# Kernel optimization log

Hardware: AMD Instinct MI355X
Metric: run time of the kernel (lower is better)

Reference implementation:

```python
import jax, jax.numpy as jnp
import numpy as np

B, CQ, CKV, LQ, LKV, HEADS = 4, 1024, 1024, 2048, 2048, 16


def _conv1x1(W, x):
    # Conv1d with kernel size 1: out[b,o,l] = sum_i W[o,i] * x[b,i,l]
    return jnp.einsum('oi,bil->bol', W, x)


def _linear_interp(x, L_out):
    # F.interpolate(mode='linear', align_corners=False) on (B,C,L)
    B_, C_, L_in = x.shape
    if L_in == L_out:
        return x
    scale = L_in / L_out
    pos = (jnp.arange(L_out, dtype=x.dtype) + 0.5) * scale - 0.5
    pos = jnp.clip(pos, 0.0, L_in - 1)
    lo = jnp.floor(pos).astype(jnp.int32)
    hi = jnp.minimum(lo + 1, L_in - 1)
    w = (pos - lo.astype(x.dtype))
    return x[:, :, lo] * (1.0 - w) + x[:, :, hi] * w


def setup_inputs() -> dict:
    key = jax.random.key(0)
    ks = jax.random.split(key, 7)
    winit = 1.0 / np.sqrt(CQ)
    return {
        'query': jax.random.normal(ks[0], (B, CQ, LQ), dtype=jnp.float32),
        'context': jax.random.normal(ks[1], (B, CKV, LKV), dtype=jnp.float32),
        'Wq': jax.random.normal(ks[2], (CQ, CQ), dtype=jnp.float32) * winit,
        'Wk': jax.random.normal(ks[3], (CQ, CKV), dtype=jnp.float32) * winit,
        'Wv': jax.random.normal(ks[4], (CQ, CKV), dtype=jnp.float32) * winit,
        'Wo': jax.random.normal(ks[5], (CQ, CQ), dtype=jnp.float32) * winit,
        'bo': jnp.zeros((CQ,), dtype=jnp.float32),
        'heads': HEADS,
    }


def reference(query, context, Wq, Wk, Wv, Wo, bo, heads):
    B_, Cq, Lq = query.shape
    H = heads
    D = Cq // H
    scale = D ** (-0.5)
    q = _conv1x1(Wq, query).reshape(B_, H, D, Lq)
    k = _conv1x1(Wk, context)
    v = _conv1x1(Wv, context)
    if k.shape[2] != Lq:
        k = _linear_interp(k, Lq)
        v = _linear_interp(v, Lq)
    k = k.reshape(B_, H, D, Lq)
    v = v.reshape(B_, H, D, Lq)
    attn = jnp.einsum('bhdi,bhdj->bhij', q, k) * scale
    attn = jax.nn.softmax(attn, axis=-1)
    out = jnp.einsum('bhij,bhdj->bhdi', attn, v).reshape(B_, Cq, Lq)
    return _conv1x1(Wo, out) + bo[None, :, None] + query
```

## Files before the change

### kernel.cpp

```cpp
#include <hip/hip_runtime.h>
#include <hip/hip_bf16.h>

typedef __bf16 bf16;
typedef __attribute__((ext_vector_type(8))) __bf16 bf16x8;
typedef __attribute__((ext_vector_type(4))) __bf16 bf16x4;
typedef __attribute__((ext_vector_type(4))) float f32x4;
typedef __attribute__((ext_vector_type(8))) float f32x8;
typedef __attribute__((ext_vector_type(16))) float f32x16;
typedef unsigned int uint2v __attribute__((ext_vector_type(2)));

#define B_ 4
#define C_ 1024
#define L_ 2048
#define H_ 16
#define D_ 64

__device__ __forceinline__ int swz(int row, int g) {
    return row * 64 + (((g ^ row) & 7) << 3);
}

__device__ __forceinline__ void async_ld16(const bf16* g, bf16* l) {
    __builtin_amdgcn_global_load_lds(
        (const __attribute__((address_space(1))) unsigned int*)g,
        (__attribute__((address_space(3))) unsigned int*)l, 16, 0, 0);
}

__device__ __forceinline__ float fast_exp2(float x) {
    float r;
    asm("v_exp_f32 %0, %1" : "=v"(r) : "v"(x));
    return r;
}

__global__ void cvt_w4(const float* __restrict__ wq, const float* __restrict__ wk,
                       const float* __restrict__ wv, const float* __restrict__ wo,
                       bf16* __restrict__ oq, bf16* __restrict__ ok,
                       bf16* __restrict__ ov, bf16* __restrict__ oo,
                       float qscale) {
    int z = blockIdx.y;
    const float* in = (z == 0) ? wq : (z == 1) ? wk : (z == 2) ? wv : wo;
    bf16* out       = (z == 0) ? oq : (z == 1) ? ok : (z == 2) ? ov : oo;
    float scale     = (z == 0) ? qscale : 1.0f;
    int i = (blockIdx.x * blockDim.x + threadIdx.x) * 4;
    f32x4 x = *(const f32x4*)&in[i];
    bf16x4 y;
#pragma unroll
    for (int e = 0; e < 4; e++) y[e] = (bf16)(x[e] * scale);
    *(bf16x4*)&out[i] = y;
}

__global__ void transpose_cvt2(const float* __restrict__ q,
                               const float* __restrict__ c,
                               bf16* __restrict__ qo, bf16* __restrict__ co,
                               int nb) {
    __shared__ bf16 s[32][33];
    int z  = blockIdx.z;
    const float* pin;
    bf16* pout;
    if (z < nb) { pin = q + (size_t)z * C_ * L_;        pout = qo + (size_t)z * L_ * C_; }
    else        { pin = c + (size_t)(z - nb) * C_ * L_; pout = co + (size_t)(z - nb) * L_ * C_; }
    int c0 = blockIdx.x * 32;
    int r0 = blockIdx.y * 32;
#pragma unroll
    for (int k = 0; k < 4; k++) {
        int r = r0 + threadIdx.y + k * 8;
        s[threadIdx.y + k * 8][threadIdx.x] = (bf16)pin[(size_t)r * L_ + c0 + threadIdx.x];
    }
    __syncthreads();
#pragma unroll
    for (int k = 0; k < 4; k++) {
        int cc = c0 + threadIdx.y + k * 8;
        pout[(size_t)cc * C_ + r0 + threadIdx.x] = s[threadIdx.x][threadIdx.y + k * 8];
    }
}

__global__ __launch_bounds__(256) void gemm_fused3(const bf16* __restrict__ qT,
                                                   const bf16* __restrict__ ctxT,
                                                   const bf16* __restrict__ Wq,
                                                   const bf16* __restrict__ Wk,
                                                   const bf16* __restrict__ Wv,
                                                   bf16* __restrict__ qP,
                                                   bf16* __restrict__ kP,
                                                   bf16* __restrict__ vP,
                                                   int nb) {
    __shared__ __align__(16) bf16 smem[4 * 128 * 64];

    int seg = blockIdx.y;
    int r   = blockIdx.x;
    int cpx = nb << 4;
    int lg  = (r & 7) * cpx + (r >> 3);

    const bf16 *aP, *bP;
    bf16* dP;
    int S;
    if (seg == 0) {
        int m_idx = lg >> 3, n_idx = lg & 7;
        aP = qT + (size_t)m_idx * 128 * C_;
        bP = Wq + (size_t)n_idx * 128 * C_;
        dP = qP + (size_t)m_idx * 128 * C_ + n_idx * 128;
        S = C_;
    } else if (seg == 1) {
        int m_idx = lg >> 3, n_idx = lg & 7;
        aP = ctxT + (size_t)m_idx * 128 * C_;
        bP = Wk + (size_t)n_idx * 128 * C_;
        dP = kP + (size_t)m_idx * 128 * C_ + n_idx * 128;
        S = C_;
    } else {
        int m_idx = lg & 7;
        int nt    = lg >> 3;
        int zb    = nt >> 4;
        int nc0   = (nt & 15) * 128;
        aP = Wv + (size_t)m_idx * 128 * C_;
        bP = ctxT + (size_t)nt * 128 * C_;
        dP = vP + (size_t)zb * C_ * L_ + (size_t)m_idx * 128 * L_ + nc0;
        S = L_;
    }

    int t = threadIdx.x;
    int lane = t & 63, wave = t >> 6;
    int l15 = lane & 15, quad = lane >> 4;
    int wm = (wave >> 1) * 64, wn = (wave & 1) * 64;

    f32x4 acc[4][4];
#pragma unroll
    for (int i = 0; i < 4; i++)
#pragma unroll
        for (int j = 0; j < 4; j++) {
            f32x4 z = {0.f, 0.f, 0.f, 0.f};
            acc[i][j] = z;
        }

    int r8 = lane >> 3;
    int gl = (((lane & 7) ^ r8) & 7) * 8;
    const bf16* aG = aP + (size_t)(wave * 32 + r8) * C_ + gl;
    const bf16* wG = bP + (size_t)(wave * 32 + r8) * C_ + gl;

    auto STAGE = [&](int buf, int kk) {
        bf16* Ab = smem + buf * 8192;
        bf16* Wb = smem + 16384 + buf * 8192;
#pragma unroll
        for (int p = 0; p < 4; p++) {
            async_ld16(aG + kk + (size_t)p * 8 * C_, &Ab[(wave * 32 + p * 8) * 64]);
            async_ld16(wG + kk + (size_t)p * 8 * C_, &Wb[(wave * 32 + p * 8) * 64]);
        }
    };

    STAGE(0, 0);
    const int KT = C_ >> 6;
    for (int it = 0; it < KT; ++it) {
        int cur = it & 1;
        if (it + 1 < KT) {
            STAGE(cur ^ 1, (it + 1) << 6);
            asm volatile("s_waitcnt vmcnt(8)" ::: "memory");
        } else {
            asm volatile("s_waitcnt vmcnt(0)" ::: "memory");
        }
        __builtin_amdgcn_s_barrier();
        asm volatile("" ::: "memory");
        const bf16* Ab = smem + cur * 8192;
        const bf16* Wb = smem + 16384 + cur * 8192;
#pragma unroll
        for (int ks = 0; ks < 2; ks++) {
            bf16x8 af[4], bfr[4];
#pragma unroll
            for (int i = 0; i < 4; i++)
                af[i] = *(const bf16x8*)&Ab[swz(wm + i * 16 + l15, ks * 4 + quad)];
#pragma unroll
            for (int i = 0; i < 4; i++)
                bfr[i] = *(const bf16x8*)&Wb[swz(wn + i * 16 + l15, ks * 4 + quad)];
#pragma unroll
            for (int mt = 0; mt < 4; mt++)
#pragma unroll
                for (int nt2 = 0; nt2 < 4; nt2++)
                    acc[mt][nt2] = __builtin_amdgcn_mfma_f32_16x16x32_bf16(
                        af[mt], bfr[nt2], acc[mt][nt2], 0, 0, 0);
        }
        asm volatile("" ::: "memory");
        __builtin_amdgcn_s_barrier();
    }
    __syncthreads();

    bf16 (*Ts2)[136] = (bf16 (*)[136])smem;
#pragma unroll
    for (int mt = 0; mt < 4; mt++)
#pragma unroll
        for (int nt2 = 0; nt2 < 4; nt2++)
#pragma unroll
            for (int rr = 0; rr < 4; rr++)
                Ts2[wm + mt * 16 + quad * 4 + rr][wn + nt2 * 16 + l15] =
                    (bf16)acc[mt][nt2][rr];
    __syncthreads();
#pragma unroll
    for (int j = 0; j < 8; j++) {
        int idx = t + 256 * j;
        int ml  = idx >> 4;
        int nl8 = (idx & 15) * 8;
        bf16x8 x = *(const bf16x8*)&Ts2[ml][nl8];
        *(bf16x8*)&dP[(size_t)ml * S + nl8] = x;
    }
}

__global__ __launch_bounds__(256) void gemm_o_final(const bf16* __restrict__ A_,
                                                    const bf16* __restrict__ Wt,
                                                    const float* __restrict__ query_,
                                                    const float* __restrict__ bo,
                                                    float* __restrict__ out_,
                                                    int nb) {
    __shared__ __align__(16) bf16 smem[4 * 128 * 64];

    int bid = blockIdx.x;
    int cpx = nb << 4;
    int lg  = (bid & 7) * cpx + (bid >> 3);
    int m   = lg >> 3;
    int n0  = (lg & 7) * 128;
    int zb  = m >> 4;
    int l0  = (m & 15) * 128;

    const bf16* A      = A_ + (size_t)m * 128 * C_;
    const float* query = query_ + (size_t)zb * C_ * L_;
    float* out         = out_   + (size_t)zb * C_ * L_;

    int t = threadIdx.x;
    int lane = t & 63, wave = t >> 6;
    int l15 = lane & 15, quad = lane >> 4;
    int wm = (wave >> 1) * 64, wn = (wave & 1) * 64;

    f32x4 acc[4][4];
#pragma unroll
    for (int i = 0; i < 4; i++)
#pragma unroll
        for (int j = 0; j < 4; j++) {
            f32x4 z = {0.f, 0.f, 0.f, 0.f};
            acc[i][j] = z;
        }

    int r8 = lane >> 3;
    int gl = (((lane & 7) ^ r8) & 7) * 8;
    const bf16* aG = A  + (size_t)(wave * 32 + r8) * C_ + gl;
    const bf16* wG = Wt + (size_t)(n0 + wave * 32 + r8) * C_ + gl;

    auto STAGE = [&](int buf, int kk) {
        bf16* Ab = smem + buf * 8192;
        bf16* Wb = smem + 16384 + buf * 8192;
#pragma unroll
        for (int p = 0; p < 4; p++) {
            async_ld16(aG + kk + (size_t)p * 8 * C_, &Ab[(wave * 32 + p * 8) * 64]);
            async_ld16(wG + kk + (size_t)p * 8 * C_, &Wb[(wave * 32 + p * 8) * 64]);
        }
    };

    STAGE(0, 0);
    const int KT = C_ >> 6;
    for (int it = 0; it < KT; ++it) {
        int cur = it & 1;
        if (it + 1 < KT) {
            STAGE(cur ^ 1, (it + 1) << 6);
            asm volatile("s_waitcnt vmcnt(8)" ::: "memory");
        } else {
            asm volatile("s_waitcnt vmcnt(0)" ::: "memory");
        }
        __builtin_amdgcn_s_barrier();
        asm volatile("" ::: "memory");
        const bf16* Ab = smem + cur * 8192;
        const bf16* Wb = smem + 16384 + cur * 8192;
#pragma unroll
        for (int ks = 0; ks < 2; ks++) {
            bf16x8 af[4], bfr[4];
#pragma unroll
            for (int i = 0; i < 4; i++)
                af[i] = *(const bf16x8*)&Ab[swz(wm + i * 16 + l15, ks * 4 + quad)];
#pragma unroll
            for (int i = 0; i < 4; i++)
                bfr[i] = *(const bf16x8*)&Wb[swz(wn + i * 16 + l15, ks * 4 + quad)];
#pragma unroll
            for (int mt = 0; mt < 4; mt++)
#pragma unroll
                for (int nt = 0; nt < 4; nt++)
                    acc[mt][nt] = __builtin_amdgcn_mfma_f32_16x16x32_bf16(
                        af[mt], bfr[nt], acc[mt][nt], 0, 0, 0);
        }
        asm volatile("" ::: "memory");
        __builtin_amdgcn_s_barrier();
    }
    __syncthreads();

    bf16 (*Ts)[136] = (bf16 (*)[136])smem;
#pragma unroll
    for (int mt = 0; mt < 4; mt++)
#pragma unroll
        for (int nt = 0; nt < 4; nt++)
#pragma unroll
            for (int rr = 0; rr < 4; rr++)
                Ts[wn + nt * 16 + l15][wm + mt * 16 + quad * 4 + rr] = (bf16)acc[mt][nt][rr];
    __syncthreads();
#pragma unroll
    for (int j = 0; j < 8; j++) {
        int idx = t + 256 * j;
        int cl  = idx >> 4;
        int ll8 = (idx & 15) * 8;
        int c   = n0 + cl;
        size_t goff = (size_t)c * L_ + l0 + ll8;
        bf16x8 y = *(const bf16x8*)&Ts[cl][ll8];
        f32x8 q = *(const f32x8*)&query[goff];
        float bias = bo[c];
        f32x8 o;
#pragma unroll
        for (int e = 0; e < 8; e++)
            o[e] = (float)y[e] + bias + q[e];
        *(f32x8*)&out[goff] = o;
    }
}

__global__ __launch_bounds__(256) void flash_attn(const bf16* qT,
                                                  const bf16* __restrict__ kT,
                                                  const bf16* __restrict__ v,
                                                  bf16* oT) {
    __shared__ __align__(16) bf16 Ks[3][64 * 64];
    __shared__ __align__(16) bf16 Vs[3][64 * 64];
    int bid = blockIdx.x;
    int cpx = gridDim.x >> 3;
    int logical = (bid & 7) * cpx + (bid >> 3);
    int i0 = (logical & 15) * 128;
    int g  = logical >> 4;
    int h  = g & 15;
    int zb = g >> 4;
    int t = threadIdx.x, lane = t & 63, wave = t >> 6;
    int l31 = lane & 31, kh = lane >> 5;

    const bf16* qB = qT + (size_t)zb * L_ * C_ + (size_t)h * D_;
    const bf16* kB = kT + (size_t)zb * L_ * C_ + (size_t)h * D_;
    const bf16* vB = v  + (size_t)zb * C_ * L_ + (size_t)h * D_ * L_;
    bf16* oB       = oT + (size_t)zb * L_ * C_ + (size_t)h * D_;

    bf16x8 qf[4];
#pragma unroll
    for (int kt = 0; kt < 4; kt++)
        qf[kt] = *(const bf16x8*)&qB[(size_t)(i0 + wave * 32 + l31) * C_ +
                                     kt * 16 + kh * 8];

    f32x16 acc_o[2];
#pragma unroll
    for (int dt = 0; dt < 2; dt++)
#pragma unroll
        for (int r = 0; r < 16; r++) acc_o[dt][r] = 0.f;
    f32x16 acc_l;
#pragma unroll
    for (int r = 0; r < 16; r++) acc_l[r] = 0.f;
    f32x16 z16;
#pragma unroll
    for (int r = 0; r < 16; r++) z16[r] = 0.f;

    bf16x8 onesf;
#pragma unroll
    for (int e = 0; e < 8; e++) onesf[e] = (bf16)1.0f;

    int r8 = lane >> 3;
    int gl = (((lane & 7) ^ r8) & 7) * 8;
    const bf16* kG = kB + (size_t)(wave * 16 + r8) * C_ + gl;
    const bf16* vG = vB + (size_t)(wave * 16 + r8) * L_ + gl;

    auto STAGE = [&](int buf, int j0n) {
#pragma unroll
        for (int p = 0; p < 2; p++) {
            async_ld16(kG + (size_t)j0n * C_ + (size_t)p * 8 * C_,
                       &Ks[buf][(wave * 16 + p * 8) * 64]);
            async_ld16(vG + j0n + (size_t)p * 8 * L_,
                       &Vs[buf][(wave * 16 + p * 8) * 64]);
        }
    };

    STAGE(0, 0);
    STAGE(1, 64);

    const int NT = L_ / 64;
    int cur = 0, sb = 2;
    for (int it = 0; it < NT; ++it) {
        if (it + 2 < NT) {
            STAGE(sb, (it + 2) * 64);
            asm volatile("s_waitcnt vmcnt(8)" ::: "memory");
        } else if (it + 1 < NT) {
            asm volatile("s_waitcnt vmcnt(4)" ::: "memory");
        } else {
            asm volatile("s_waitcnt vmcnt(0)" ::: "memory");
        }
        __builtin_amdgcn_s_barrier();
        asm volatile("" ::: "memory");

        const bf16* kb = &Ks[cur][0];
        const bf16* vb = &Vs[cur][0];

#pragma unroll
        for (int jt = 0; jt < 2; jt++) {
            f32x16 s;
            {
                bf16x8 a = *(const bf16x8*)&kb[swz(jt * 32 + l31, kh)];
                s = __builtin_amdgcn_mfma_f32_32x32x16_bf16(a, qf[0], z16, 0, 0, 0);
            }
#pragma unroll
            for (int kt = 1; kt < 4; kt++) {
                bf16x8 a = *(const bf16x8*)&kb[swz(jt * 32 + l31, kt * 2 + kh)];
                s = __builtin_amdgcn_mfma_f32_32x32x16_bf16(a, qf[kt], s, 0, 0, 0);
            }
            unsigned w[4][2];
#pragma unroll
            for (int q = 0; q < 4; q++)
#pragma unroll
                for (int c = 0; c < 2; c++) {
                    float p0 = fast_exp2(s[q * 4 + 2 * c]);
                    float p1 = fast_exp2(s[q * 4 + 2 * c + 1]);
                    asm("v_cvt_pk_bf16_f32 %0, %1, %2"
                        : "=v"(w[q][c]) : "v"(p0), "v"(p1));
                }
#pragma unroll
            for (int kp = 0; kp < 2; kp++) {
                int ks = jt * 2 + kp;
                uint2v r0 = __builtin_amdgcn_permlane32_swap(
                    w[kp * 2][0], w[kp * 2 + 1][0], false, false);
                uint2v r1 = __builtin_amdgcn_permlane32_swap(
                    w[kp * 2][1], w[kp * 2 + 1][1], false, false);
                union { unsigned u[4]; bf16x8 v8; } af;
                af.u[0] = r0[0]; af.u[1] = r1[0];
                af.u[2] = r0[1]; af.u[3] = r1[1];
#pragma unroll
                for (int dt = 0; dt < 2; dt++) {
                    bf16x8 b = *(const bf16x8*)&vb[swz(dt * 32 + l31, ks * 2 + kh)];
                    acc_o[dt] = __builtin_amdgcn_mfma_f32_32x32x16_bf16(
                        af.v8, b, acc_o[dt], 0, 0, 0);
                }
                acc_l = __builtin_amdgcn_mfma_f32_32x32x16_bf16(
                    af.v8, onesf, acc_l, 0, 0, 0);
            }
        }
        asm volatile("" ::: "memory");
        __builtin_amdgcn_s_barrier();
        cur = (cur == 2) ? 0 : cur + 1;
        sb  = (sb  == 2) ? 0 : sb  + 1;
    }

    float inv[16];
#pragma unroll
    for (int r = 0; r < 16; r++) inv[r] = __builtin_amdgcn_rcpf(acc_l[r]);
#pragma unroll
    for (int dt = 0; dt < 2; dt++)
#pragma unroll
        for (int q = 0; q < 4; q++)
#pragma unroll
            for (int r = 0; r < 4; r++) {
                int row = i0 + wave * 32 + 8 * q + 4 * kh + r;
                oB[(size_t)row * C_ + dt * 32 + l31] =
                    (bf16)(acc_o[dt][q * 4 + r] * inv[q * 4 + r]);
            }
}

extern "C" void kernel_launch(void* const* d_in, const int* in_sizes, int n_in,
                              void* d_out, int out_size, void* d_ws, size_t ws_size,
                              hipStream_t stream) {
    const float* query   = (const float*)d_in[0];
    const float* context = (const float*)d_in[1];
    const float* Wq = (const float*)d_in[2];
    const float* Wk = (const float*)d_in[3];
    const float* Wv = (const float*)d_in[4];
    const float* Wo = (const float*)d_in[5];
    const float* bo = (const float*)d_in[6];
    float* out = (float*)d_out;

    const size_t Sw = (size_t)C_ * C_;
    size_t need_batched = (4 * Sw + 3 * (size_t)B_ * L_ * C_) * sizeof(bf16);
    int nb = (ws_size >= need_batched) ? B_ : 1;

    const size_t Sslot = (size_t)nb * L_ * C_;
    bf16* WqB = (bf16*)d_ws;
    bf16* WkB = WqB + Sw;
    bf16* WvB = WkB + Sw;
    bf16* WoB = WvB + Sw;
    bf16* slotA = WoB + Sw;
    bf16* slotB = slotA + Sslot;
    bf16* slotC = slotB + Sslot;

    cvt_w4<<<dim3((unsigned)(Sw / 4 / 256), 4), 256, 0, stream>>>(
        Wq, Wk, Wv, Wo, WqB, WkB, WvB, WoB, 0.1803368801111204f);

    dim3 tb(32, 8);

    for (int b0 = 0; b0 < B_; b0 += nb) {
        const float* qx = query   + (size_t)b0 * C_ * L_;
        const float* cx = context + (size_t)b0 * C_ * L_;
        float* ob       = out     + (size_t)b0 * C_ * L_;

        bf16* vscr  = (bf16*)ob;
        bf16* ctxTs = (bf16*)ob + Sslot;

        transpose_cvt2<<<dim3(L_ / 32, C_ / 32, 2 * nb), tb, 0, stream>>>(
            qx, cx, slotA, ctxTs, nb);
        gemm_fused3<<<dim3(128 * nb, 3), 256, 0, stream>>>(
            slotA, ctxTs, WqB, WkB, WvB, slotB, slotC, vscr, nb);
        flash_attn<<<256 * nb, 256, 0, stream>>>(slotB, slotC, vscr, slotB);
        gemm_o_final<<<128 * nb, 256, 0, stream>>>(slotB, WoB, qx, bo, ob, nb);
    }
}
```

Before: 309.9 us.

## Software-pipeline QK of next tile with softmax-PV of current tile

Restructures the attention inner loop so the QK^T MFMAs for tile it+1 are issued before the exp/convert/PV work for tile it, using double-buffered score registers and an unrolled-by-two loop. Raises wave priority during the QK phase with s_setprio. The aim is to overlap transcendental and permute work with matrix-core work and so hide MFMA latency. It costs extra VGPRs for a second score buffer, which may lower occupancy, and it changes the wait counts and buffer rotation in the three-stage LDS ring.

```diff
diff --git a/kernel.cpp b/kernel.cpp
--- a/kernel.cpp
+++ b/kernel.cpp
@@ -368,26 +368,7 @@
         }
     };
 
-    STAGE(0, 0);
-    STAGE(1, 64);
-
-    const int NT = L_ / 64;
-    int cur = 0, sb = 2;
-    for (int it = 0; it < NT; ++it) {
-        if (it + 2 < NT) {
-            STAGE(sb, (it + 2) * 64);
-            asm volatile("s_waitcnt vmcnt(8)" ::: "memory");
-        } else if (it + 1 < NT) {
-            asm volatile("s_waitcnt vmcnt(4)" ::: "memory");
-        } else {
-            asm volatile("s_waitcnt vmcnt(0)" ::: "memory");
-        }
-        __builtin_amdgcn_s_barrier();
-        asm volatile("" ::: "memory");
-
-        const bf16* kb = &Ks[cur][0];
-        const bf16* vb = &Vs[cur][0];
-
+    auto QK = [&](const bf16* kb, f32x16* sout) {
 #pragma unroll
         for (int jt = 0; jt < 2; jt++) {
             f32x16 s;
@@ -400,13 +381,20 @@
                 bf16x8 a = *(const bf16x8*)&kb[swz(jt * 32 + l31, kt * 2 + kh)];
                 s = __builtin_amdgcn_mfma_f32_32x32x16_bf16(a, qf[kt], s, 0, 0, 0);
             }
+            sout[jt] = s;
+        }
+    };
+
+    auto SMPV = [&](const f32x16* sin, const bf16* vb) {
+#pragma unroll
+        for (int jt = 0; jt < 2; jt++) {
             unsigned w[4][2];
 #pragma unroll
             for (int q = 0; q < 4; q++)
 #pragma unroll
                 for (int c = 0; c < 2; c++) {
-                    float p0 = fast_exp2(s[q * 4 + 2 * c]);
-                    float p1 = fast_exp2(s[q * 4 + 2 * c + 1]);
+                    float p0 = fast_exp2(sin[jt][q * 4 + 2 * c]);
+                    float p1 = fast_exp2(sin[jt][q * 4 + 2 * c + 1]);
                     asm("v_cvt_pk_bf16_f32 %0, %1, %2"
                         : "=v"(w[q][c]) : "v"(p0), "v"(p1));
                 }
@@ -430,11 +418,48 @@
                     af.v8, onesf, acc_l, 0, 0, 0);
             }
         }
-        asm volatile("" ::: "memory");
-        __builtin_amdgcn_s_barrier();
-        cur = (cur == 2) ? 0 : cur + 1;
-        sb  = (sb  == 2) ? 0 : sb  + 1;
-    }
+    };
+
+    const int NT = L_ / 64;
+    f32x16 sb0[2], sb1[2];
+
+    STAGE(0, 0);
+    STAGE(1, 64);
+    asm volatile("s_waitcnt vmcnt(4)" ::: "memory");
+    __builtin_amdgcn_s_barrier();
+    asm volatile("" ::: "memory");
+    QK(&Ks[0][0], sb0);
+
+    int cb = 0, nbf = 1, sbf = 2;
+    auto TILE_FULL = [&](int it, f32x16* scur, f32x16* snext) {
+        STAGE(sbf, (it + 2) * 64);
+        asm volatile("s_waitcnt vmcnt(4)" ::: "memory");
+        __builtin_amdgcn_s_barrier();
+        asm volatile("" ::: "memory");
+        __builtin_amdgcn_s_setprio(1);
+        QK(&Ks[nbf][0], snext);
+        __builtin_amdgcn_s_setprio(0);
+        SMPV(scur, &Vs[cb][0]);
+        asm volatile("" ::: "memory");
+        __builtin_amdgcn_s_barrier();
+        int t0 = cb; cb = nbf; nbf = sbf; sbf = t0;
+    };
+
+    for (int it = 0; it < NT - 2; it += 2) {
+        TILE_FULL(it, sb0, sb1);
+        TILE_FULL(it + 1, sb1, sb0);
+    }
+    {
+        asm volatile("s_waitcnt vmcnt(0)" ::: "memory");
+        __builtin_amdgcn_s_barrier();
+        asm volatile("" ::: "memory");
+        __builtin_amdgcn_s_setprio(1);
+        QK(&Ks[nbf][0], sb1);
+        __builtin_amdgcn_s_setprio(0);
+        SMPV(sb0, &Vs[cb][0]);
+        int t0 = cb; cb = nbf; nbf = sbf; sbf = t0;
+    }
+    SMPV(sb1, &Vs[cb][0]);
 
     float inv[16];
 #pragma unroll
```

Result: faster. 296.3 us (-4.4%).

## Process 64 query rows per wave in flash attention, double-buffer K/V

Applied to the files above, without the earlier changes.

Each wave now handles two 32-row query tiles instead of one, so every K/V fragment read from LDS feeds twice as many MFMAs. Each block covers 256 query rows and the grid is halved to 128 blocks per batch. The K/V ring shrinks from three buffers to two, and the next stage is issued after the end-of-iteration barrier. This cuts LDS and global K/V traffic per FLOP, at the cost of more registers, fewer blocks (512 total) and a shorter prefetch distance.

```diff
diff --git a/kernel.cpp b/kernel.cpp
--- a/kernel.cpp
+++ b/kernel.cpp
@@ -314,13 +314,13 @@
                                                   const bf16* __restrict__ kT,
                                                   const bf16* __restrict__ v,
                                                   bf16* oT) {
-    __shared__ __align__(16) bf16 Ks[3][64 * 64];
-    __shared__ __align__(16) bf16 Vs[3][64 * 64];
+    __shared__ __align__(16) bf16 Ks[2][64 * 64];
+    __shared__ __align__(16) bf16 Vs[2][64 * 64];
     int bid = blockIdx.x;
     int cpx = gridDim.x >> 3;
     int logical = (bid & 7) * cpx + (bid >> 3);
-    int i0 = (logical & 15) * 128;
-    int g  = logical >> 4;
+    int i0 = (logical & 7) * 256;
+    int g  = logical >> 3;
     int h  = g & 15;
     int zb = g >> 4;
     int t = threadIdx.x, lane = t & 63, wave = t >> 6;
@@ -331,20 +331,23 @@
     const bf16* vB = v  + (size_t)zb * C_ * L_ + (size_t)h * D_ * L_;
     bf16* oB       = oT + (size_t)zb * L_ * C_ + (size_t)h * D_;
 
-    bf16x8 qf[4];
-#pragma unroll
-    for (int kt = 0; kt < 4; kt++)
-        qf[kt] = *(const bf16x8*)&qB[(size_t)(i0 + wave * 32 + l31) * C_ +
-                                     kt * 16 + kh * 8];
-
-    f32x16 acc_o[2];
+    bf16x8 qf0[4], qf1[4];
+#pragma unroll
+    for (int kt = 0; kt < 4; kt++) {
+        qf0[kt] = *(const bf16x8*)&qB[(size_t)(i0 + wave * 64 + l31) * C_ +
+                                      kt * 16 + kh * 8];
+        qf1[kt] = *(const bf16x8*)&qB[(size_t)(i0 + wave * 64 + 32 + l31) * C_ +
+                                      kt * 16 + kh * 8];
+    }
+
+    f32x16 acc_o0[2], acc_o1[2];
 #pragma unroll
     for (int dt = 0; dt < 2; dt++)
 #pragma unroll
-        for (int r = 0; r < 16; r++) acc_o[dt][r] = 0.f;
-    f32x16 acc_l;
-#pragma unroll
-    for (int r = 0; r < 16; r++) acc_l[r] = 0.f;
+        for (int r = 0; r < 16; r++) { acc_o0[dt][r] = 0.f; acc_o1[dt][r] = 0.f; }
+    f32x16 acc_l0, acc_l1;
+#pragma unroll
+    for (int r = 0; r < 16; r++) { acc_l0[r] = 0.f; acc_l1[r] = 0.f; }
     f32x16 z16;
 #pragma unroll
     for (int r = 0; r < 16; r++) z16[r] = 0.f;
@@ -359,25 +362,19 @@
     const bf16* vG = vB + (size_t)(wave * 16 + r8) * L_ + gl;
 
     auto STAGE = [&](int buf, int j0n) {
-#pragma unroll
-        for (int p = 0; p < 2; p++) {
-            async_ld16(kG + (size_t)j0n * C_ + (size_t)p * 8 * C_,
-                       &Ks[buf][(wave * 16 + p * 8) * 64]);
-            async_ld16(vG + j0n + (size_t)p * 8 * L_,
-                       &Vs[buf][(wave * 16 + p * 8) * 64]);
-        }
+        async_ld16(kG + (size_t)j0n * C_,          &Ks[buf][(wave * 16) * 64]);
+        async_ld16(kG + (size_t)j0n * C_ + 8 * C_, &Ks[buf][(wave * 16 + 8) * 64]);
+        async_ld16(vG + j0n,                       &Vs[buf][(wave * 16) * 64]);
+        async_ld16(vG + j0n + (size_t)8 * L_,      &Vs[buf][(wave * 16 + 8) * 64]);
     };
+
+    const int NT = L_ / 64;
 
     STAGE(0, 0);
     STAGE(1, 64);
 
-    const int NT = L_ / 64;
-    int cur = 0, sb = 2;
     for (int it = 0; it < NT; ++it) {
-        if (it + 2 < NT) {
-            STAGE(sb, (it + 2) * 64);
-            asm volatile("s_waitcnt vmcnt(8)" ::: "memory");
-        } else if (it + 1 < NT) {
+        if (it + 1 < NT) {
             asm volatile("s_waitcnt vmcnt(4)" ::: "memory");
         } else {
             asm volatile("s_waitcnt vmcnt(0)" ::: "memory");
@@ -385,69 +382,91 @@
         __builtin_amdgcn_s_barrier();
         asm volatile("" ::: "memory");
 
-        const bf16* kb = &Ks[cur][0];
-        const bf16* vb = &Vs[cur][0];
+        const bf16* kb = &Ks[it & 1][0];
+        const bf16* vb = &Vs[it & 1][0];
 
 #pragma unroll
         for (int jt = 0; jt < 2; jt++) {
-            f32x16 s;
+            f32x16 s0, s1;
             {
                 bf16x8 a = *(const bf16x8*)&kb[swz(jt * 32 + l31, kh)];
-                s = __builtin_amdgcn_mfma_f32_32x32x16_bf16(a, qf[0], z16, 0, 0, 0);
+                s0 = __builtin_amdgcn_mfma_f32_32x32x16_bf16(a, qf0[0], z16, 0, 0, 0);
+                s1 = __builtin_amdgcn_mfma_f32_32x32x16_bf16(a, qf1[0], z16, 0, 0, 0);
             }
 #pragma unroll
             for (int kt = 1; kt < 4; kt++) {
                 bf16x8 a = *(const bf16x8*)&kb[swz(jt * 32 + l31, kt * 2 + kh)];
-                s = __builtin_amdgcn_mfma_f32_32x32x16_bf16(a, qf[kt], s, 0, 0, 0);
+                s0 = __builtin_amdgcn_mfma_f32_32x32x16_bf16(a, qf0[kt], s0, 0, 0, 0);
+                s1 = __builtin_amdgcn_mfma_f32_32x32x16_bf16(a, qf1[kt], s1, 0, 0, 0);
             }
-            unsigned w[4][2];
+            unsigned w0[4][2], w1[4][2];
 #pragma unroll
             for (int q = 0; q < 4; q++)
 #pragma unroll
                 for (int c = 0; c < 2; c++) {
-                    float p0 = fast_exp2(s[q * 4 + 2 * c]);
-                    float p1 = fast_exp2(s[q * 4 + 2 * c + 1]);
+                    float a0 = fast_exp2(s0[q * 4 + 2 * c]);
+                    float a1 = fast_exp2(s0[q * 4 + 2 * c + 1]);
                     asm("v_cvt_pk_bf16_f32 %0, %1, %2"
-                        : "=v"(w[q][c]) : "v"(p0), "v"(p1));
+                        : "=v"(w0[q][c]) : "v"(a0), "v"(a1));
+                    float b0 = fast_exp2(s1[q * 4 + 2 * c]);
+                    float b1 = fast_exp2(s1[q * 4 + 2 * c + 1]);
+                    asm("v_cvt_pk_bf16_f32 %0, %1, %2"
+                        : "=v"(w1[q][c]) : "v"(b0), "v"(b1));
                 }
 #pragma unroll
             for (int kp = 0; kp < 2; kp++) {
                 int ks = jt * 2 + kp;
-                uint2v r0 = __builtin_amdgcn_permlane32_swap(
-                    w[kp * 2][0], w[kp * 2 + 1][0], false, false);
-                uint2v r1 = __builtin_amdgcn_permlane32_swap(
-                    w[kp * 2][1], w[kp * 2 + 1][1], false, false);
-                union { unsigned u[4]; bf16x8 v8; } af;
-                af.u[0] = r0[0]; af.u[1] = r1[0];
-                af.u[2] = r0[1]; af.u[3] = r1[1];
+                uint2v r0a = __builtin_amdgcn_permlane32_swap(
+                    w0[kp * 2][0], w0[kp * 2 + 1][0], false, false);
+                uint2v r1a = __builtin_amdgcn_permlane32_swap(
+                    w0[kp * 2][1], w0[kp * 2 + 1][1], false, false);
+                uint2v r0b = __builtin_amdgcn_permlane32_swap(
+                    w1[kp * 2][0], w1[kp * 2 + 1][0], false, false);
+                uint2v r1b = __builtin_amdgcn_permlane32_swap(
+                    w1[kp * 2][1], w1[kp * 2 + 1][1], false, false);
+                union { unsigned u[4]; bf16x8 v8; } af0, af1;
+                af0.u[0] = r0a[0]; af0.u[1] = r1a[0];
+                af0.u[2] = r0a[1]; af0.u[3] = r1a[1];
+                af1.u[0] = r0b[0]; af1.u[1] = r1b[0];
+                af1.u[2] = r0b[1]; af1.u[3] = r1b[1];
 #pragma unroll
                 for (int dt = 0; dt < 2; dt++) {
                     bf16x8 b = *(const bf16x8*)&vb[swz(dt * 32 + l31, ks * 2 + kh)];
-                    acc_o[dt] = __builtin_amdgcn_mfma_f32_32x32x16_bf16(
-                        af.v8, b, acc_o[dt], 0, 0, 0);
+                    acc_o0[dt] = __builtin_amdgcn_mfma_f32_32x32x16_bf16(
+                        af0.v8, b, acc_o0[dt], 0, 0, 0);
+                    acc_o1[dt] = __builtin_amdgcn_mfma_f32_32x32x16_bf16(
+                        af1.v8, b, acc_o1[dt], 0, 0, 0);
                 }
-                acc_l = __builtin_amdgcn_mfma_f32_32x32x16_bf16(
-                    af.v8, onesf, acc_l, 0, 0, 0);
+                acc_l0 = __builtin_amdgcn_mfma_f32_32x32x16_bf16(
+                    af0.v8, onesf, acc_l0, 0, 0, 0);
+                acc_l1 = __builtin_amdgcn_mfma_f32_32x32x16_bf16(
+                    af1.v8, onesf, acc_l1, 0, 0, 0);
             }
         }
         asm volatile("" ::: "memory");
         __builtin_amdgcn_s_barrier();
-        cur = (cur == 2) ? 0 : cur + 1;
-        sb  = (sb  == 2) ? 0 : sb  + 1;
-    }
-
-    float inv[16];
-#pragma unroll
-    for (int r = 0; r < 16; r++) inv[r] = __builtin_amdgcn_rcpf(acc_l[r]);
+        if (it + 2 < NT) STAGE(it & 1, (it + 2) * 64);
+    }
+
+    float inv0[16], inv1[16];
+#pragma unroll
+    for (int r = 0; r < 16; r++) {
+        inv0[r] = __builtin_amdgcn_rcpf(acc_l0[r]);
+        inv1[r] = __builtin_amdgcn_rcpf(acc_l1[r]);
+    }
 #pragma unroll
     for (int dt = 0; dt < 2; dt++)
 #pragma unroll
         for (int q = 0; q < 4; q++)
 #pragma unroll
             for (int r = 0; r < 4; r++) {
-                int row = i0 + wave * 32 + 8 * q + 4 * kh + r;
-                oB[(size_t)row * C_ + dt * 32 + l31] =
-                    (bf16)(acc_o[dt][q * 4 + r] * inv[q * 4 + r]);
+                int rl = 8 * q + 4 * kh + r;
+                int row0 = i0 + wave * 64 + rl;
+                oB[(size_t)row0 * C_ + dt * 32 + l31] =
+                    (bf16)(acc_o0[dt][q * 4 + r] * inv0[q * 4 + r]);
+                int row1 = i0 + wave * 64 + 32 + rl;
+                oB[(size_t)row1 * C_ + dt * 32 + l31] =
+                    (bf16)(acc_o1[dt][q * 4 + r] * inv1[q * 4 + r]);
             }
 }
 
@@ -493,7 +512,7 @@
             qx, cx, slotA, ctxTs, nb);
         gemm_fused3<<<dim3(128 * nb, 3), 256, 0, stream>>>(
             slotA, ctxTs, WqB, WkB, WvB, slotB, slotC, vscr, nb);
-        flash_attn<<<256 * nb, 256, 0, stream>>>(slotB, slotC, vscr, slotB);
+        flash_attn<<<128 * nb, 256, 0, stream>>>(slotB, slotC, vscr, slotB);
         gemm_o_final<<<128 * nb, 256, 0, stream>>>(slotB, WoB, qx, bo, ob, nb);
     }
 }
```

Result: faster. 300.7 us (-2.9%).
